# Performance work log

Hardware: AMD Instinct MI355X
Metric: run time of the kernel (lower is better)

Reference implementation:

```python
import jax, jax.numpy as jnp
import numpy as np
import math

B, S, D, H = 2, 2048, 1024, 16
HD = D // H
WINDOW_LEFT = 256   # window_size=(256,-1): only left constraint active
NEG = -1e9


def rotate_half(x):
    x1, x2 = jnp.split(x, 2, axis=-1)
    return jnp.concatenate([-x2, x1], axis=-1)


def setup_inputs() -> dict:
    key = jax.random.key(0)
    ks = jax.random.split(key, 10)
    x = jax.random.normal(ks[0], (B, S, D), dtype=jnp.float32)
    mask = jnp.ones((B, S), dtype=bool)
    cos = jax.random.uniform(ks[1], (B, S, HD), dtype=jnp.float32)
    sin = jax.random.uniform(ks[2], (B, S, HD), dtype=jnp.float32)
    sc = 1.0 / math.sqrt(D)
    Wq = jax.random.normal(ks[3], (D, D), dtype=jnp.float32) * sc
    bq = jax.random.normal(ks[4], (D,), dtype=jnp.float32) * 0.02
    Wk = jax.random.normal(ks[5], (D, D), dtype=jnp.float32) * sc
    Wv = jax.random.normal(ks[6], (D, D), dtype=jnp.float32) * sc
    bv = jax.random.normal(ks[7], (D,), dtype=jnp.float32) * 0.02
    Wo = jax.random.normal(ks[8], (D, D), dtype=jnp.float32) * sc
    bo = jax.random.normal(ks[9], (D,), dtype=jnp.float32) * 0.02
    return {"x": x, "mask": mask, "cos": cos, "sin": sin,
            "Wq": Wq, "bq": bq, "Wk": Wk, "Wv": Wv, "bv": bv,
            "Wo": Wo, "bo": bo}


def reference(x, mask, cos, sin, Wq, bq, Wk, Wv, bv, Wo, bo):
    batch, seq_len, embed_dim = x.shape
    scale = 1.0 / math.sqrt(HD)

    q = x @ Wq + bq          # [b,s,d], bias on q
    k = x @ Wk               # no bias on k
    v = x @ Wv + bv          # bias on v

    def split_heads(t):
        return jnp.swapaxes(t.reshape(batch, seq_len, H, HD), 1, 2)  # [b,h,s,hd]

    q, k, v = split_heads(q), split_heads(k), split_heads(v)

    c = cos[:, None, :, :]   # [b,1,s,hd]
    s_ = sin[:, None, :, :]
    q = q * c + rotate_half(q) * s_
    k = k * c + rotate_half(k) * s_

    scores = jnp.einsum('bhqd,bhkd->bhqk', q, k) * scale
    # padding mask over keys
    scores = jnp.where(mask[:, None, None, :], scores, NEG)
    # causal + sliding-window (left=256) masks combined
    pos = jnp.arange(seq_len)
    rel = pos[None, :] - pos[:, None]          # k - q
    keep = (rel <= 0) & (rel >= -WINDOW_LEFT)  # causal AND window-left
    scores = jnp.where(keep, scores, NEG)

    weights = jax.nn.softmax(scores, axis=-1)
    context = jnp.einsum('bhqk,bhkd->bhqd', weights, v)
    context = jnp.swapaxes(context, 1, 2).reshape(batch, seq_len, embed_dim)
    out = context @ Wo + bo
    out = out * mask[..., None]
    return out
```

## Files before the change

kernel.cpp:

```cpp
#include <hip/hip_runtime.h>
#include <cstdint>
#include <cstddef>

typedef __bf16 bf16;
typedef bf16 bf16x4 __attribute__((ext_vector_type(4)));
typedef bf16 bf16x8 __attribute__((ext_vector_type(8)));
typedef float f32x4 __attribute__((ext_vector_type(4)));

#define S_LEN 2048
#define DIM   1024
#define NHEAD 16
#define HDIM  64

__device__ __forceinline__ f32x4 mfma16(bf16x8 a, bf16x8 b, f32x4 c) {
    return __builtin_amdgcn_mfma_f32_16x16x32_bf16(a, b, c, 0, 0, 0);
}

__device__ __forceinline__ float exp2fast(float x) {
    return __builtin_amdgcn_exp2f(x);
}

__device__ __forceinline__ void gload_lds16(const bf16* g, bf16* l) {
    __builtin_amdgcn_global_load_lds(
        (const __attribute__((address_space(1))) unsigned*)g,
        (__attribute__((address_space(3))) unsigned*)l, 16, 0, 0);
}

__global__ __launch_bounds__(256) void cvt_x_kernel(const float* __restrict__ x,
                                                    bf16* __restrict__ xb) {
    int i = blockIdx.x * 256 + threadIdx.x;
    float4 v = ((const float4*)x)[i];
    bf16x4 o = { (bf16)v.x, (bf16)v.y, (bf16)v.z, (bf16)v.w };
    ((bf16x4*)xb)[i] = o;
}

__global__ __launch_bounds__(256) void wt_kernel(const float* __restrict__ Wq, const float* __restrict__ Wk,
                                                 const float* __restrict__ Wv, const float* __restrict__ Wo,
                                                 bf16* __restrict__ WqT, bf16* __restrict__ WkT,
                                                 bf16* __restrict__ WvT, bf16* __restrict__ WoT) {
    const float* W; bf16* WT;
    int z = blockIdx.z;
    if      (z == 0) { W = Wq; WT = WqT; }
    else if (z == 1) { W = Wk; WT = WkT; }
    else if (z == 2) { W = Wv; WT = WvT; }
    else             { W = Wo; WT = WoT; }
    __shared__ bf16 tile[64][72];
    int k0 = blockIdx.x * 64, n0 = blockIdx.y * 64;
    int t = threadIdx.x;
#pragma unroll
    for (int p = 0; p < 4; ++p) {
        int task = p * 256 + t;
        int ki = task >> 4, nj = (task & 15) * 4;
        float4 v = *(const float4*)(W + (size_t)(k0 + ki) * DIM + n0 + nj);
        tile[ki][nj + 0] = (bf16)v.x; tile[ki][nj + 1] = (bf16)v.y;
        tile[ki][nj + 2] = (bf16)v.z; tile[ki][nj + 3] = (bf16)v.w;
    }
    __syncthreads();
#pragma unroll
    for (int p = 0; p < 4; ++p) {
        int task = p * 256 + t;
        int ni = task >> 4, kj = (task & 15) * 4;
        bf16x4 o = { tile[kj + 0][ni], tile[kj + 1][ni], tile[kj + 2][ni], tile[kj + 3][ni] };
        *(bf16x4*)(WT + (size_t)(n0 + ni) * DIM + k0 + kj) = o;
    }
}

__device__ __forceinline__ void stage_tile(const bf16* __restrict__ A, const bf16* __restrict__ BT,
                                           int m0, int n0, int k0,
                                           bf16* sA, bf16* sB, int w, int lane) {
#pragma unroll
    for (int p = 0; p < 2; ++p) {
        int c = p * 256 + w * 64 + lane;
        const bf16* ga = A + (size_t)(m0 + (c >> 2)) * DIM + k0 + (c & 3) * 8;
        gload_lds16(ga, sA + (p * 256 + w * 64) * 8);
        const bf16* gb = BT + (size_t)(n0 + (c >> 2)) * DIM + k0 + (c & 3) * 8;
        gload_lds16(gb, sB + (p * 256 + w * 64) * 8);
    }
}

__device__ __forceinline__ void gemm_main(const bf16* __restrict__ A, const bf16* __restrict__ BT,
                                          int m0, int n0, f32x4 acc[4][4]) {
    __shared__ bf16 sA[3][128 * 32];
    __shared__ bf16 sB[3][128 * 32];
    int t = threadIdx.x;
    int lane = t & 63, w = t >> 6;
    int wr = w >> 1, wc = w & 1;
    int lc = lane & 15, lr = lane >> 4;
    const int NSTEP = DIM / 32;

    stage_tile(A, BT, m0, n0, 0,  sA[0], sB[0], w, lane);
    stage_tile(A, BT, m0, n0, 32, sA[1], sB[1], w, lane);

    int rs = 0, ss = 2;
    for (int kt = 0; kt < NSTEP; ++kt) {
        if (kt < NSTEP - 1) asm volatile("s_waitcnt vmcnt(4)" ::: "memory");
        else                asm volatile("s_waitcnt vmcnt(0)" ::: "memory");
        __builtin_amdgcn_s_barrier();
        asm volatile("" ::: "memory");
        if (kt < NSTEP - 2)
            stage_tile(A, BT, m0, n0, (kt + 2) * 32, sA[ss], sB[ss], w, lane);

        const bf16* pa = sA[rs] + (wr * 64 + lc) * 32 + lr * 8;
        const bf16* pb = sB[rs] + (wc * 64 + lc) * 32 + lr * 8;
        bf16x8 af[4], bfr[4];
#pragma unroll
        for (int m = 0; m < 4; ++m) af[m] = *(const bf16x8*)(pa + m * 16 * 32);
#pragma unroll
        for (int n = 0; n < 4; ++n) bfr[n] = *(const bf16x8*)(pb + n * 16 * 32);
#pragma unroll
        for (int m = 0; m < 4; ++m)
#pragma unroll
            for (int n = 0; n < 4; ++n)
                acc[m][n] = mfma16(af[m], bfr[n], acc[m][n]);
        rs = (rs == 2) ? 0 : rs + 1;
        ss = (ss == 2) ? 0 : ss + 1;
    }
}

__global__ __launch_bounds__(256, 3) void gemm_qkv_kernel(const bf16* __restrict__ xb,
                                                          const bf16* __restrict__ WqT, const bf16* __restrict__ WkT,
                                                          const bf16* __restrict__ WvT,
                                                          const float* __restrict__ bq, const float* __restrict__ bv,
                                                          const float* __restrict__ cosp, const float* __restrict__ sinp,
                                                          bf16* __restrict__ qT, bf16* __restrict__ kT,
                                                          bf16* __restrict__ vT) {
    int z = blockIdx.z;
    const bf16* BT = (z == 0) ? WqT : (z == 1) ? WkT : WvT;
    int m0 = blockIdx.x * 128, n0 = blockIdx.y * 128;
    f32x4 acc[4][4] = {};
    gemm_main(xb, BT, m0, n0, acc);

    int t = threadIdx.x;
    int lane = t & 63, w = t >> 6;
    int wr = w >> 1, wc = w & 1;
    int lc = lane & 15, lr = lane >> 4;
    int row0 = m0 + wr * 64 + lr * 4;
    int h = (n0 >> 6) + wc;

    if (z < 2) {
        bf16* qkT = (z == 0) ? qT : kT;
#pragma unroll
        for (int nf = 0; nf < 2; ++nf) {
            int hd1 = lc + nf * 16;
            int c1i = h * HDIM + hd1;
            float b1 = (z == 0) ? bq[c1i] : 0.0f;
            float b2 = (z == 0) ? bq[c1i + 32] : 0.0f;
#pragma unroll
            for (int mf = 0; mf < 4; ++mf) {
#pragma unroll
                for (int r = 0; r < 4; ++r) {
                    int bs = row0 + mf * 16 + r;
                    size_t cb = (size_t)bs * HDIM + hd1;
                    float c1 = cosp[cb], s1 = sinp[cb];
                    float c2 = cosp[cb + 32], s2 = sinp[cb + 32];
                    float v1 = acc[mf][nf][r] + b1;
                    float v2 = acc[mf][nf + 2][r] + b2;
                    int b = bs >> 11, s = bs & (S_LEN - 1);
                    size_t o = ((size_t)(b * NHEAD + h) * S_LEN + s) * HDIM;
                    qkT[o + hd1]      = (bf16)(v1 * c1 - v2 * s1);
                    qkT[o + hd1 + 32] = (bf16)(v2 * c2 + v1 * s2);
                }
            }
        }
    } else {
#pragma unroll
        for (int nf = 0; nf < 4; ++nf) {
            int hd = lc + nf * 16;
            float bvv = bv[h * HDIM + hd];
#pragma unroll
            for (int mf = 0; mf < 4; ++mf) {
                bf16x4 o;
#pragma unroll
                for (int r = 0; r < 4; ++r) o[r] = (bf16)(acc[mf][nf][r] + bvv);
                int bs = row0 + mf * 16;
                int b = bs >> 11, s = bs & (S_LEN - 1);
                *(bf16x4*)(vT + ((size_t)((b * NHEAD + h) * HDIM + hd)) * S_LEN + s) = o;
            }
        }
    }
}

__global__ __launch_bounds__(256, 3) void gemm_out_kernel(const bf16* __restrict__ ctx, const bf16* __restrict__ WoT,
                                                          const float* __restrict__ bo, float* __restrict__ out) {
    int m0 = blockIdx.x * 128, n0 = blockIdx.y * 128;
    f32x4 acc[4][4] = {};
    gemm_main(ctx, WoT, m0, n0, acc);
    int t = threadIdx.x;
    int lane = t & 63, w = t >> 6;
    int wr = w >> 1, wc = w & 1;
    int lc = lane & 15, lr = lane >> 4;
    int row0 = m0 + wr * 64 + lr * 4;
    int col0 = n0 + wc * 64 + lc;
#pragma unroll
    for (int nf = 0; nf < 4; ++nf) {
        int col = col0 + nf * 16;
        float bvv = bo[col];
#pragma unroll
        for (int mf = 0; mf < 4; ++mf)
#pragma unroll
            for (int r = 0; r < 4; ++r)
                out[(size_t)(row0 + mf * 16 + r) * DIM + col] = acc[mf][nf][r] + bvv;
    }
}

__global__ __launch_bounds__(64) void attn_kernel(const bf16* __restrict__ qT, const bf16* __restrict__ kT,
                                                  const bf16* __restrict__ vT, bf16* __restrict__ ctx) {
    int q0 = blockIdx.x * 32;
    int bh = blockIdx.y;
    int b = bh >> 4, h = bh & 15;
    int lane = threadIdx.x;
    int lc = lane & 15, lr = lane >> 4;
    __shared__ bf16 sP[32 * 64];
    char* sPb = (char*)sP;
    const bf16* Qb = qT + (size_t)bh * S_LEN * HDIM;
    const bf16* Kb = kT + (size_t)bh * S_LEN * HDIM;
    const bf16* Vb = vT + (size_t)bh * HDIM * S_LEN;

    const float SCL = 0.125f * 1.44269504089f;
    const int swz = (lc & 7) << 4;

    bf16x8 qf[2][2];
#pragma unroll
    for (int mf = 0; mf < 2; ++mf)
#pragma unroll
        for (int kk = 0; kk < 2; ++kk)
            qf[mf][kk] = *(const bf16x8*)(Qb + (size_t)(q0 + mf * 16 + lc) * HDIM + kk * 32 + lr * 8);

    f32x4 accO[2][4] = {};
    float mrun[2] = { -30000.0f, -30000.0f };
    float lrun[2] = { 0.0f, 0.0f };

    int klo = (q0 >= 256) ? ((q0 - 256) >> 6) : 0;
    int khi = (q0 + 31) >> 6;

    bf16x8 kfc[8], kfn[8], vf[8];
#pragma unroll
    for (int nf = 0; nf < 4; ++nf)
#pragma unroll
        for (int kk = 0; kk < 2; ++kk)
            kfc[nf * 2 + kk] = *(const bf16x8*)(Kb + (size_t)(klo * 64 + nf * 16 + lc) * HDIM + kk * 32 + lr * 8);

    for (int kt = klo; kt <= khi; ++kt) {
        int kbase = kt * 64;
#pragma unroll
        for (int n4 = 0; n4 < 4; ++n4)
#pragma unroll
            for (int kk = 0; kk < 2; ++kk)
                vf[n4 * 2 + kk] = *(const bf16x8*)(Vb + (size_t)(n4 * 16 + lc) * S_LEN + kbase + kk * 32 + lr * 8);
        if (kt < khi) {
#pragma unroll
            for (int nf = 0; nf < 4; ++nf)
#pragma unroll
                for (int kk = 0; kk < 2; ++kk)
                    kfn[nf * 2 + kk] = *(const bf16x8*)(Kb + (size_t)(kbase + 64 + nf * 16 + lc) * HDIM + kk * 32 + lr * 8);
        }

        f32x4 sacc[2][4] = {};
        __builtin_amdgcn_s_setprio(1);
#pragma unroll
        for (int nf = 0; nf < 4; ++nf)
#pragma unroll
            for (int kk = 0; kk < 2; ++kk) {
                sacc[0][nf] = mfma16(kfc[nf * 2 + kk], qf[0][kk], sacc[0][nf]);
                sacc[1][nf] = mfma16(kfc[nf * 2 + kk], qf[1][kk], sacc[1][nf]);
            }
        __builtin_amdgcn_s_setprio(0);
#pragma unroll
        for (int mf = 0; mf < 2; ++mf) {
            int qi = q0 + mf * 16 + lc;
#pragma unroll
            for (int nf = 0; nf < 4; ++nf)
#pragma unroll
                for (int r = 0; r < 4; ++r) {
                    int ki = kbase + nf * 16 + lr * 4 + r;
                    bool keep = (ki <= qi) && (ki >= qi - 256);
                    sacc[mf][nf][r] = keep ? sacc[mf][nf][r] * SCL : -30000.0f;
                }
        }
#pragma unroll
        for (int mf = 0; mf < 2; ++mf) {
            float mx = sacc[mf][0][0];
#pragma unroll
            for (int nf = 0; nf < 4; ++nf)
#pragma unroll
                for (int r = 0; r < 4; ++r) mx = fmaxf(mx, sacc[mf][nf][r]);
            mx = fmaxf(mx, __shfl_xor(mx, 16));
            mx = fmaxf(mx, __shfl_xor(mx, 32));
            float mnew = fmaxf(mrun[mf], mx);
            float alpha = exp2fast(mrun[mf] - mnew);
            mrun[mf] = mnew;
            float rsum = 0.0f;
#pragma unroll
            for (int nf = 0; nf < 4; ++nf)
#pragma unroll
                for (int r = 0; r < 4; ++r) {
                    float e = exp2fast(sacc[mf][nf][r] - mnew);
                    sacc[mf][nf][r] = e;
                    rsum += e;
                }
            rsum += __shfl_xor(rsum, 16);
            rsum += __shfl_xor(rsum, 32);
            lrun[mf] = lrun[mf] * alpha + rsum;
            float aq[4];
#pragma unroll
            for (int r = 0; r < 4; ++r) aq[r] = __shfl(alpha, lr * 4 + r);
#pragma unroll
            for (int n4 = 0; n4 < 4; ++n4)
#pragma unroll
                for (int r = 0; r < 4; ++r) accO[mf][n4][r] *= aq[r];
        }
#pragma unroll
        for (int mf = 0; mf < 2; ++mf)
#pragma unroll
            for (int nf = 0; nf < 4; ++nf) {
                bf16x4 o = { (bf16)sacc[mf][nf][0], (bf16)sacc[mf][nf][1],
                             (bf16)sacc[mf][nf][2], (bf16)sacc[mf][nf][3] };
                int wb = ((mf * 16 + lc) * 64 + nf * 16 + lr * 4) * 2;
                *(bf16x4*)(sPb + (wb ^ swz)) = o;
            }
        asm volatile("s_waitcnt lgkmcnt(0)" ::: "memory");
        bf16x8 pf[2][2];
#pragma unroll
        for (int mf = 0; mf < 2; ++mf)
#pragma unroll
            for (int kk = 0; kk < 2; ++kk) {
                int rb = ((mf * 16 + lc) * 64 + kk * 32 + lr * 8) * 2;
                pf[mf][kk] = *(const bf16x8*)(sPb + (rb ^ swz));
            }
        __builtin_amdgcn_s_setprio(1);
#pragma unroll
        for (int n4 = 0; n4 < 4; ++n4)
#pragma unroll
            for (int kk = 0; kk < 2; ++kk) {
                accO[0][n4] = mfma16(pf[0][kk], vf[n4 * 2 + kk], accO[0][n4]);
                accO[1][n4] = mfma16(pf[1][kk], vf[n4 * 2 + kk], accO[1][n4]);
            }
        __builtin_amdgcn_s_setprio(0);
#pragma unroll
        for (int i = 0; i < 8; ++i) kfc[i] = kfn[i];
    }
#pragma unroll
    for (int mf = 0; mf < 2; ++mf) {
        float linv = 1.0f / lrun[mf];
        float lq[4];
#pragma unroll
        for (int r = 0; r < 4; ++r) lq[r] = __shfl(linv, lr * 4 + r);
#pragma unroll
        for (int n4 = 0; n4 < 4; ++n4)
#pragma unroll
            for (int r = 0; r < 4; ++r) {
                int s = q0 + mf * 16 + lr * 4 + r;
                int d = n4 * 16 + lc;
                ctx[((size_t)(b * S_LEN + s)) * DIM + h * HDIM + d] = (bf16)(accO[mf][n4][r] * lq[r]);
            }
    }
}

extern "C" void kernel_launch(void* const* d_in, const int* in_sizes, int n_in,
                              void* d_out, int out_size, void* d_ws, size_t ws_size,
                              hipStream_t stream) {
    const float* x    = (const float*)d_in[0];
    const float* cosp = (const float*)d_in[2];
    const float* sinp = (const float*)d_in[3];
    const float* Wq   = (const float*)d_in[4];
    const float* bq   = (const float*)d_in[5];
    const float* Wk   = (const float*)d_in[6];
    const float* Wv   = (const float*)d_in[7];
    const float* bv   = (const float*)d_in[8];
    const float* Wo   = (const float*)d_in[9];
    const float* bo   = (const float*)d_in[10];
    float* out = (float*)d_out;

    char* ws = (char*)d_ws;
    const size_t MB = 1ull << 20;
    bf16* xb  = (bf16*)(ws + 0 * MB);
    bf16* WqT = (bf16*)(ws + 8 * MB);
    bf16* WkT = (bf16*)(ws + 10 * MB);
    bf16* WvT = (bf16*)(ws + 12 * MB);
    bf16* WoT = (bf16*)(ws + 14 * MB);
    bf16* qT  = (bf16*)(ws + 16 * MB);
    bf16* kT  = (bf16*)(ws + 24 * MB);
    bf16* vT  = (bf16*)(ws + 32 * MB);
    bf16* ctx = (bf16*)(ws + 40 * MB);

    cvt_x_kernel<<<4096, 256, 0, stream>>>(x, xb);
    wt_kernel<<<dim3(16, 16, 4), 256, 0, stream>>>(Wq, Wk, Wv, Wo, WqT, WkT, WvT, WoT);
    gemm_qkv_kernel<<<dim3(32, 8, 3), 256, 0, stream>>>(xb, WqT, WkT, WvT, bq, bv, cosp, sinp, qT, kT, vT);
    attn_kernel<<<dim3(64, 32), 64, 0, stream>>>(qT, kT, vT, ctx);
    gemm_out_kernel<<<dim3(32, 8), 256, 0, stream>>>(ctx, WoT, bo, out);
}
```

Measured before the change: 104.6 us.

## Rewrite QKV GEMM with 256x256 tiles, swizzled LDS and block remap

Replaces the fused QKV projection GEMM's 128x128 tile with 256-thread blocks by a 256x256 tile with 512 threads. It uses a K-step of 64, double-buffered LDS with an XOR swizzle, a remapped 1D grid of 192 blocks, and s_setprio around MFMA bursts. Wq/Wk/Wv are treated as one contiguous transposed weight, which relies on WqT/WkT/WvT sitting adjacent in the workspace. The aim is more data reuse per tile, fewer LDS bank conflicts and better L2 locality. The cost is higher register pressure (128 accumulator floats per thread), a grid smaller than the CU count, and one full wait plus barrier per K step.

Result: no change. 103.9 us (-0.6%).

```diff
diff --git a/kernel.cpp b/kernel.cpp
--- a/kernel.cpp
+++ b/kernel.cpp
@@ -65,88 +65,94 @@
     }
 }
 
-__device__ __forceinline__ void stage_tile(const bf16* __restrict__ A, const bf16* __restrict__ BT,
-                                           int m0, int n0, int k0,
-                                           bf16* sA, bf16* sB, int w, int lane) {
-#pragma unroll
-    for (int p = 0; p < 2; ++p) {
-        int c = p * 256 + w * 64 + lane;
-        const bf16* ga = A + (size_t)(m0 + (c >> 2)) * DIM + k0 + (c & 3) * 8;
-        gload_lds16(ga, sA + (p * 256 + w * 64) * 8);
-        const bf16* gb = BT + (size_t)(n0 + (c >> 2)) * DIM + k0 + (c & 3) * 8;
-        gload_lds16(gb, sB + (p * 256 + w * 64) * 8);
-    }
-}
-
-__device__ __forceinline__ void gemm_main(const bf16* __restrict__ A, const bf16* __restrict__ BT,
-                                          int m0, int n0, f32x4 acc[4][4]) {
-    __shared__ bf16 sA[3][128 * 32];
-    __shared__ bf16 sB[3][128 * 32];
-    int t = threadIdx.x;
-    int lane = t & 63, w = t >> 6;
-    int wr = w >> 1, wc = w & 1;
-    int lc = lane & 15, lr = lane >> 4;
-    const int NSTEP = DIM / 32;
-
-    stage_tile(A, BT, m0, n0, 0,  sA[0], sB[0], w, lane);
-    stage_tile(A, BT, m0, n0, 32, sA[1], sB[1], w, lane);
-
-    int rs = 0, ss = 2;
-    for (int kt = 0; kt < NSTEP; ++kt) {
-        if (kt < NSTEP - 1) asm volatile("s_waitcnt vmcnt(4)" ::: "memory");
-        else                asm volatile("s_waitcnt vmcnt(0)" ::: "memory");
-        __builtin_amdgcn_s_barrier();
-        asm volatile("" ::: "memory");
-        if (kt < NSTEP - 2)
-            stage_tile(A, BT, m0, n0, (kt + 2) * 32, sA[ss], sB[ss], w, lane);
-
-        const bf16* pa = sA[rs] + (wr * 64 + lc) * 32 + lr * 8;
-        const bf16* pb = sB[rs] + (wc * 64 + lc) * 32 + lr * 8;
-        bf16x8 af[4], bfr[4];
-#pragma unroll
-        for (int m = 0; m < 4; ++m) af[m] = *(const bf16x8*)(pa + m * 16 * 32);
-#pragma unroll
-        for (int n = 0; n < 4; ++n) bfr[n] = *(const bf16x8*)(pb + n * 16 * 32);
-#pragma unroll
-        for (int m = 0; m < 4; ++m)
-#pragma unroll
-            for (int n = 0; n < 4; ++n)
-                acc[m][n] = mfma16(af[m], bfr[n], acc[m][n]);
-        rs = (rs == 2) ? 0 : rs + 1;
-        ss = (ss == 2) ? 0 : ss + 1;
-    }
-}
-
-__global__ __launch_bounds__(256, 3) void gemm_qkv_kernel(const bf16* __restrict__ xb,
-                                                          const bf16* __restrict__ WqT, const bf16* __restrict__ WkT,
-                                                          const bf16* __restrict__ WvT,
+__device__ __forceinline__ void stage256(const bf16* __restrict__ A, const bf16* __restrict__ BT,
+                                         int m0, int n0, int k0, int t, int w, bf16* dst) {
+#pragma unroll
+    for (int i = 0; i < 4; ++i) {
+        int c = i * 512 + t;
+        int row = c >> 3;
+        int colb = ((c & 7) * 16) ^ ((row & 7) << 4);
+        gload_lds16(A + (size_t)(m0 + row) * DIM + k0 + (colb >> 1), dst + i * 4096 + w * 512);
+    }
+#pragma unroll
+    for (int i = 0; i < 4; ++i) {
+        int c = i * 512 + t;
+        int row = c >> 3;
+        int colb = ((c & 7) * 16) ^ ((row & 7) << 4);
+        gload_lds16(BT + (size_t)(n0 + row) * DIM + k0 + (colb >> 1), dst + 16384 + i * 4096 + w * 512);
+    }
+}
+
+__global__ __launch_bounds__(512, 2) void gemm_qkv_kernel(const bf16* __restrict__ xb,
+                                                          const bf16* __restrict__ WallT,
                                                           const float* __restrict__ bq, const float* __restrict__ bv,
                                                           const float* __restrict__ cosp, const float* __restrict__ sinp,
                                                           bf16* __restrict__ qT, bf16* __restrict__ kT,
                                                           bf16* __restrict__ vT) {
-    int z = blockIdx.z;
-    const bf16* BT = (z == 0) ? WqT : (z == 1) ? WkT : WvT;
-    int m0 = blockIdx.x * 128, n0 = blockIdx.y * 128;
-    f32x4 acc[4][4] = {};
-    gemm_main(xb, BT, m0, n0, acc);
-
-    int t = threadIdx.x;
-    int lane = t & 63, w = t >> 6;
-    int wr = w >> 1, wc = w & 1;
+    __shared__ bf16 lds[2][32768];
+    int t = threadIdx.x, lane = t & 63, w = t >> 6;
+    int wr = w >> 2, wc = w & 3;
     int lc = lane & 15, lr = lane >> 4;
-    int row0 = m0 + wr * 64 + lr * 4;
-    int h = (n0 >> 6) + wc;
-
+    int bid = blockIdx.x;
+    int swz = (bid & 7) * 24 + (bid >> 3);
+    int bx = swz / 12, by = swz % 12;
+    int m0 = bx * 256, n0 = by * 256;
+
+    f32x4 acc[8][4] = {};
+    const int aswz = (lc & 7) << 4;
+
+    stage256(xb, WallT, m0, n0, 0, t, w, lds[0]);
+    asm volatile("s_waitcnt vmcnt(0)" ::: "memory");
+    __builtin_amdgcn_s_barrier();
+    __builtin_amdgcn_sched_barrier(0);
+
+    const int NT = DIM / 64;
+    for (int kt = 0; kt < NT; ++kt) {
+        if (kt + 1 < NT) stage256(xb, WallT, m0, n0, (kt + 1) * 64, t, w, lds[(kt + 1) & 1]);
+        const char* bufb = (const char*)lds[kt & 1];
+        bf16x8 aF[4], bF[4];
+#pragma unroll
+        for (int ks = 0; ks < 2; ++ks) {
+#pragma unroll
+            for (int nf = 0; nf < 4; ++nf) {
+                int row = wc * 64 + nf * 16 + lc;
+                bF[nf] = *(const bf16x8*)(bufb + 32768 + ((row * 128 + ks * 64 + lr * 16) ^ aswz));
+            }
+#pragma unroll
+            for (int half = 0; half < 2; ++half) {
+#pragma unroll
+                for (int m4 = 0; m4 < 4; ++m4) {
+                    int row = wr * 128 + (half * 4 + m4) * 16 + lc;
+                    aF[m4] = *(const bf16x8*)(bufb + ((row * 128 + ks * 64 + lr * 16) ^ aswz));
+                }
+                __builtin_amdgcn_s_setprio(1);
+#pragma unroll
+                for (int m4 = 0; m4 < 4; ++m4)
+#pragma unroll
+                    for (int nf = 0; nf < 4; ++nf)
+                        acc[half * 4 + m4][nf] = mfma16(aF[m4], bF[nf], acc[half * 4 + m4][nf]);
+                __builtin_amdgcn_s_setprio(0);
+            }
+        }
+        if (kt + 1 < NT) {
+            asm volatile("s_waitcnt vmcnt(0)" ::: "memory");
+            __builtin_amdgcn_s_barrier();
+            __builtin_amdgcn_sched_barrier(0);
+        }
+    }
+
+    int z = by >> 2;
+    int h = (by & 3) * 4 + wc;
+    int row0 = m0 + wr * 128 + lr * 4;
     if (z < 2) {
         bf16* qkT = (z == 0) ? qT : kT;
 #pragma unroll
         for (int nf = 0; nf < 2; ++nf) {
-            int hd1 = lc + nf * 16;
-            int c1i = h * HDIM + hd1;
-            float b1 = (z == 0) ? bq[c1i] : 0.0f;
-            float b2 = (z == 0) ? bq[c1i + 32] : 0.0f;
-#pragma unroll
-            for (int mf = 0; mf < 4; ++mf) {
+            int hd1 = nf * 16 + lc;
+            float b1 = (z == 0) ? bq[h * HDIM + hd1] : 0.0f;
+            float b2 = (z == 0) ? bq[h * HDIM + hd1 + 32] : 0.0f;
+#pragma unroll
+            for (int mf = 0; mf < 8; ++mf) {
 #pragma unroll
                 for (int r = 0; r < 4; ++r) {
                     int bs = row0 + mf * 16 + r;
@@ -165,10 +171,10 @@
     } else {
 #pragma unroll
         for (int nf = 0; nf < 4; ++nf) {
-            int hd = lc + nf * 16;
+            int hd = nf * 16 + lc;
             float bvv = bv[h * HDIM + hd];
 #pragma unroll
-            for (int mf = 0; mf < 4; ++mf) {
+            for (int mf = 0; mf < 8; ++mf) {
                 bf16x4 o;
 #pragma unroll
                 for (int r = 0; r < 4; ++r) o[r] = (bf16)(acc[mf][nf][r] + bvv);
@@ -177,6 +183,58 @@
                 *(bf16x4*)(vT + ((size_t)((b * NHEAD + h) * HDIM + hd)) * S_LEN + s) = o;
             }
         }
+    }
+}
+
+__device__ __forceinline__ void stage_tile(const bf16* __restrict__ A, const bf16* __restrict__ BT,
+                                           int m0, int n0, int k0,
+                                           bf16* sA, bf16* sB, int w, int lane) {
+#pragma unroll
+    for (int p = 0; p < 2; ++p) {
+        int c = p * 256 + w * 64 + lane;
+        const bf16* ga = A + (size_t)(m0 + (c >> 2)) * DIM + k0 + (c & 3) * 8;
+        gload_lds16(ga, sA + (p * 256 + w * 64) * 8);
+        const bf16* gb = BT + (size_t)(n0 + (c >> 2)) * DIM + k0 + (c & 3) * 8;
+        gload_lds16(gb, sB + (p * 256 + w * 64) * 8);
+    }
+}
+
+__device__ __forceinline__ void gemm_main(const bf16* __restrict__ A, const bf16* __restrict__ BT,
+                                          int m0, int n0, f32x4 acc[4][4]) {
+    __shared__ bf16 sA[3][128 * 32];
+    __shared__ bf16 sB[3][128 * 32];
+    int t = threadIdx.x;
+    int lane = t & 63, w = t >> 6;
+    int wr = w >> 1, wc = w & 1;
+    int lc = lane & 15, lr = lane >> 4;
+    const int NSTEP = DIM / 32;
+
+    stage_tile(A, BT, m0, n0, 0,  sA[0], sB[0], w, lane);
+    stage_tile(A, BT, m0, n0, 32, sA[1], sB[1], w, lane);
+
+    int rs = 0, ss = 2;
+    for (int kt = 0; kt < NSTEP; ++kt) {
+        if (kt < NSTEP - 1) asm volatile("s_waitcnt vmcnt(4)" ::: "memory");
+        else                asm volatile("s_waitcnt vmcnt(0)" ::: "memory");
+        __builtin_amdgcn_s_barrier();
+        asm volatile("" ::: "memory");
+        if (kt < NSTEP - 2)
+            stage_tile(A, BT, m0, n0, (kt + 2) * 32, sA[ss], sB[ss], w, lane);
+
+        const bf16* pa = sA[rs] + (wr * 64 + lc) * 32 + lr * 8;
+        const bf16* pb = sB[rs] + (wc * 64 + lc) * 32 + lr * 8;
+        bf16x8 af[4], bfr[4];
+#pragma unroll
+        for (int m = 0; m < 4; ++m) af[m] = *(const bf16x8*)(pa + m * 16 * 32);
+#pragma unroll
+        for (int n = 0; n < 4; ++n) bfr[n] = *(const bf16x8*)(pb + n * 16 * 32);
+#pragma unroll
+        for (int m = 0; m < 4; ++m)
+#pragma unroll
+            for (int n = 0; n < 4; ++n)
+                acc[m][n] = mfma16(af[m], bfr[n], acc[m][n]);
+        rs = (rs == 2) ? 0 : rs + 1;
+        ss = (ss == 2) ? 0 : ss + 1;
     }
 }
 
@@ -385,7 +443,7 @@
 
     cvt_x_kernel<<<4096, 256, 0, stream>>>(x, xb);
     wt_kernel<<<dim3(16, 16, 4), 256, 0, stream>>>(Wq, Wk, Wv, Wo, WqT, WkT, WvT, WoT);
-    gemm_qkv_kernel<<<dim3(32, 8, 3), 256, 0, stream>>>(xb, WqT, WkT, WvT, bq, bv, cosp, sinp, qT, kT, vT);
+    gemm_qkv_kernel<<<192, 512, 0, stream>>>(xb, WqT, bq, bv, cosp, sinp, qT, kT, vT);
     attn_kernel<<<dim3(64, 32), 64, 0, stream>>>(qT, kT, vT, ctx);
     gemm_out_kernel<<<dim3(32, 8), 256, 0, stream>>>(ctx, WoT, bo, out);
 }
```

## Swizzle QKV block order for XCD locality and retile output GEMM to 128x64

Applied to the files above, without the earlier changes.

The QKV GEMM now remaps its linear block id so that the blocks placed on each XCD (bid mod 8) form a contiguous set of output tiles, aiming for better L2 reuse of A and B tiles. The output projection GEMM gets a dedicated 128x64 tile kernel with 2 waves per block and its own triple-buffered LDS staging. This doubles the grid from 256 to 512 blocks so more CUs are busy, and applies the same XCD-aware swizzle. In exchange, each block reuses less data per tile and does more global loads per FLOP.

Result: no change. 106.0 us (+1.4%).

```diff
diff --git a/kernel.cpp b/kernel.cpp
--- a/kernel.cpp
+++ b/kernel.cpp
@@ -124,9 +124,11 @@
                                                           const float* __restrict__ cosp, const float* __restrict__ sinp,
                                                           bf16* __restrict__ qT, bf16* __restrict__ kT,
                                                           bf16* __restrict__ vT) {
-    int z = blockIdx.z;
+    int bid = blockIdx.x + 32 * blockIdx.y + 256 * blockIdx.z;
+    int wg  = (bid & 7) * 96 + (bid >> 3);
+    int z = wg >> 8, rem = wg & 255, by = rem >> 5, bx = rem & 31;
     const bf16* BT = (z == 0) ? WqT : (z == 1) ? WkT : WvT;
-    int m0 = blockIdx.x * 128, n0 = blockIdx.y * 128;
+    int m0 = bx * 128, n0 = by * 128;
     f32x4 acc[4][4] = {};
     gemm_main(xb, BT, m0, n0, acc);
 
@@ -180,20 +182,69 @@
     }
 }
 
-__global__ __launch_bounds__(256, 3) void gemm_out_kernel(const bf16* __restrict__ ctx, const bf16* __restrict__ WoT,
+__device__ __forceinline__ void stage_out(const bf16* __restrict__ A, const bf16* __restrict__ BT,
+                                          int m0, int n0, int k0,
+                                          bf16* sA, bf16* sB, int w, int t) {
+#pragma unroll
+    for (int i = 0; i < 4; ++i) {
+        int c = i * 128 + t;
+        const bf16* ga = A + (size_t)(m0 + (c >> 2)) * DIM + k0 + (c & 3) * 8;
+        gload_lds16(ga, sA + (i * 128 + w * 64) * 8);
+    }
+#pragma unroll
+    for (int i = 0; i < 2; ++i) {
+        int c = i * 128 + t;
+        const bf16* gb = BT + (size_t)(n0 + (c >> 2)) * DIM + k0 + (c & 3) * 8;
+        gload_lds16(gb, sB + (i * 128 + w * 64) * 8);
+    }
+}
+
+__global__ __launch_bounds__(128, 2) void gemm_out_kernel(const bf16* __restrict__ ctx, const bf16* __restrict__ WoT,
                                                           const float* __restrict__ bo, float* __restrict__ out) {
-    int m0 = blockIdx.x * 128, n0 = blockIdx.y * 128;
-    f32x4 acc[4][4] = {};
-    gemm_main(ctx, WoT, m0, n0, acc);
+    __shared__ bf16 sA[3][128 * 32];
+    __shared__ bf16 sB[3][64 * 32];
+    int bid = blockIdx.x + 32 * blockIdx.y;
+    int wg  = (bid & 7) * 64 + (bid >> 3);
+    int bx = wg & 31, by = wg >> 5;
+    int m0 = bx * 128, n0 = by * 64;
     int t = threadIdx.x;
     int lane = t & 63, w = t >> 6;
-    int wr = w >> 1, wc = w & 1;
     int lc = lane & 15, lr = lane >> 4;
-    int row0 = m0 + wr * 64 + lr * 4;
-    int col0 = n0 + wc * 64 + lc;
+    const int NSTEP = DIM / 32;
+
+    f32x4 acc[4][4] = {};
+    stage_out(ctx, WoT, m0, n0, 0,  sA[0], sB[0], w, t);
+    stage_out(ctx, WoT, m0, n0, 32, sA[1], sB[1], w, t);
+
+    int rs = 0, ss = 2;
+    for (int kt = 0; kt < NSTEP; ++kt) {
+        if (kt < NSTEP - 1) asm volatile("s_waitcnt vmcnt(6)" ::: "memory");
+        else                asm volatile("s_waitcnt vmcnt(0)" ::: "memory");
+        __builtin_amdgcn_s_barrier();
+        asm volatile("" ::: "memory");
+        if (kt < NSTEP - 2)
+            stage_out(ctx, WoT, m0, n0, (kt + 2) * 32, sA[ss], sB[ss], w, t);
+
+        const bf16* pa = sA[rs] + (w * 64 + lc) * 32 + lr * 8;
+        const bf16* pb = sB[rs] + lc * 32 + lr * 8;
+        bf16x8 af[4], bfr[4];
+#pragma unroll
+        for (int m = 0; m < 4; ++m) af[m] = *(const bf16x8*)(pa + m * 16 * 32);
+#pragma unroll
+        for (int n = 0; n < 4; ++n) bfr[n] = *(const bf16x8*)(pb + n * 16 * 32);
+#pragma unroll
+        for (int m = 0; m < 4; ++m)
+#pragma unroll
+            for (int n = 0; n < 4; ++n)
+                acc[m][n] = mfma16(af[m], bfr[n], acc[m][n]);
+        rs = (rs == 2) ? 0 : rs + 1;
+        ss = (ss == 2) ? 0 : ss + 1;
+    }
+
+    int row0 = m0 + w * 64 + lr * 4;
 #pragma unroll
     for (int nf = 0; nf < 4; ++nf) {
-        int col = col0 + nf * 16;
+        int col = n0 + lc + nf * 16;
         float bvv = bo[col];
 #pragma unroll
         for (int mf = 0; mf < 4; ++mf)
@@ -387,5 +438,5 @@
     wt_kernel<<<dim3(16, 16, 4), 256, 0, stream>>>(Wq, Wk, Wv, Wo, WqT, WkT, WvT, WoT);
     gemm_qkv_kernel<<<dim3(32, 8, 3), 256, 0, stream>>>(xb, WqT, WkT, WvT, bq, bv, cosp, sinp, qT, kT, vT);
     attn_kernel<<<dim3(64, 32), 64, 0, stream>>>(qT, kT, vT, ctx);
-    gemm_out_kernel<<<dim3(32, 8), 256, 0, stream>>>(ctx, WoT, bo, out);
-}
+    gemm_out_kernel<<<dim3(32, 16), 128, 0, stream>>>(ctx, WoT, bo, out);
+}
```

## Share K/V tiles across four waves via double-buffered LDS staging in attention

Applied to the files above, without the earlier changes.

The attention kernel moves from one 64-thread wave per 32-query block to 256-thread blocks covering 128 queries. K and V tiles are loaded once per block into swizzled LDS with async global-to-LDS loads and double buffering, replacing the per-wave register loads from global memory. Block IDs are remapped so each XCD handles a contiguous set of heads, which is meant to improve L2 locality. In exchange the kernel adds block-wide barriers, and some waves sit idle on tiles outside their own window, which adds work imbalance.

Result: faster. 95.45 us (-8.7%).

```diff
diff --git a/kernel.cpp b/kernel.cpp
--- a/kernel.cpp
+++ b/kernel.cpp
@@ -203,21 +203,33 @@
     }
 }
 
-__global__ __launch_bounds__(64) void attn_kernel(const bf16* __restrict__ qT, const bf16* __restrict__ kT,
-                                                  const bf16* __restrict__ vT, bf16* __restrict__ ctx) {
-    int q0 = blockIdx.x * 32;
-    int bh = blockIdx.y;
+__global__ __launch_bounds__(256, 3) void attn_kernel(const bf16* __restrict__ qT, const bf16* __restrict__ kT,
+                                                      const bf16* __restrict__ vT, bf16* __restrict__ ctx) {
+    int bid = blockIdx.x + 16 * blockIdx.y;
+    int xcd = bid & 7, idx = bid >> 3;
+    int bh = xcd * 4 + (idx >> 4);
+    int qb = idx & 15;
     int b = bh >> 4, h = bh & 15;
-    int lane = threadIdx.x;
+    int t = threadIdx.x, lane = t & 63, w = t >> 6;
     int lc = lane & 15, lr = lane >> 4;
-    __shared__ bf16 sP[32 * 64];
-    char* sPb = (char*)sP;
+
+    __shared__ bf16 sK[2][4096];
+    __shared__ bf16 sV[2][4096];
+    __shared__ bf16 sP[4][2048];
+
     const bf16* Qb = qT + (size_t)bh * S_LEN * HDIM;
     const bf16* Kb = kT + (size_t)bh * S_LEN * HDIM;
     const bf16* Vb = vT + (size_t)bh * HDIM * S_LEN;
 
     const float SCL = 0.125f * 1.44269504089f;
     const int swz = (lc & 7) << 4;
+    char* sPw = (char*)sP[w];
+
+    int q0 = qb * 128 + w * 32;
+    int kt_lo_b = (qb >= 2) ? (qb * 128 - 256) >> 6 : 0;
+    int kt_hi_b = (qb * 128 + 127) >> 6;
+    int klo_w = (q0 >= 256) ? (q0 - 256) >> 6 : 0;
+    int khi_w = (q0 + 31) >> 6;
 
     bf16x8 qf[2][2];
 #pragma unroll
@@ -230,115 +242,130 @@
     float mrun[2] = { -30000.0f, -30000.0f };
     float lrun[2] = { 0.0f, 0.0f };
 
-    int klo = (q0 >= 256) ? ((q0 - 256) >> 6) : 0;
-    int khi = (q0 + 31) >> 6;
-
-    bf16x8 kfc[8], kfn[8], vf[8];
-#pragma unroll
-    for (int nf = 0; nf < 4; ++nf)
-#pragma unroll
-        for (int kk = 0; kk < 2; ++kk)
-            kfc[nf * 2 + kk] = *(const bf16x8*)(Kb + (size_t)(klo * 64 + nf * 16 + lc) * HDIM + kk * 32 + lr * 8);
-
-    for (int kt = klo; kt <= khi; ++kt) {
-        int kbase = kt * 64;
-#pragma unroll
-        for (int n4 = 0; n4 < 4; ++n4)
-#pragma unroll
-            for (int kk = 0; kk < 2; ++kk)
-                vf[n4 * 2 + kk] = *(const bf16x8*)(Vb + (size_t)(n4 * 16 + lc) * S_LEN + kbase + kk * 32 + lr * 8);
-        if (kt < khi) {
-#pragma unroll
-            for (int nf = 0; nf < 4; ++nf)
-#pragma unroll
-                for (int kk = 0; kk < 2; ++kk)
-                    kfn[nf * 2 + kk] = *(const bf16x8*)(Kb + (size_t)(kbase + 64 + nf * 16 + lc) * HDIM + kk * 32 + lr * 8);
+#define STAGE_KV(kt_, s_) {                                                             \
+        int kbase_ = (kt_) * 64;                                                        \
+        _Pragma("unroll")                                                               \
+        for (int p = 0; p < 2; ++p) {                                                   \
+            int c = p * 256 + t;                                                        \
+            int row = c >> 3, ch = c & 7;                                               \
+            int colb = (ch * 16) ^ ((row & 7) << 4);                                    \
+            bf16* dst = (bf16*)&sK[s_][0] + (p * 256 + (t & ~63)) * 8;                  \
+            gload_lds16(Kb + (size_t)(kbase_ + row) * HDIM + (colb >> 1), dst);         \
+            bf16* dsv = (bf16*)&sV[s_][0] + (p * 256 + (t & ~63)) * 8;                  \
+            gload_lds16(Vb + (size_t)row * S_LEN + kbase_ + (colb >> 1), dsv);          \
+        }                                                                               \
+    }
+
+    STAGE_KV(kt_lo_b, 0);
+    if (kt_lo_b + 1 <= kt_hi_b) STAGE_KV(kt_lo_b + 1, 1);
+
+    for (int kt = kt_lo_b; kt <= kt_hi_b; ++kt) {
+        int s = (kt - kt_lo_b) & 1;
+        if (kt < kt_hi_b) asm volatile("s_waitcnt vmcnt(4)" ::: "memory");
+        else              asm volatile("s_waitcnt vmcnt(0)" ::: "memory");
+        __builtin_amdgcn_s_barrier();
+        asm volatile("" ::: "memory");
+
+        if (kt >= klo_w && kt <= khi_w) {
+            int kbase = kt * 64;
+            const char* kb = (const char*)&sK[s][0];
+            const char* vb = (const char*)&sV[s][0];
+
+            f32x4 sacc[2][4] = {};
+            __builtin_amdgcn_s_setprio(1);
+#pragma unroll
+            for (int nf = 0; nf < 4; ++nf) {
+                int key = nf * 16 + lc;
+#pragma unroll
+                for (int kk = 0; kk < 2; ++kk) {
+                    bf16x8 kf = *(const bf16x8*)(kb + key * 128 + ((kk * 64 + lr * 16) ^ swz));
+                    sacc[0][nf] = mfma16(kf, qf[0][kk], sacc[0][nf]);
+                    sacc[1][nf] = mfma16(kf, qf[1][kk], sacc[1][nf]);
+                }
+            }
+            __builtin_amdgcn_s_setprio(0);
+#pragma unroll
+            for (int mf = 0; mf < 2; ++mf) {
+                int qi = q0 + mf * 16 + lc;
+#pragma unroll
+                for (int nf = 0; nf < 4; ++nf)
+#pragma unroll
+                    for (int r = 0; r < 4; ++r) {
+                        int ki = kbase + nf * 16 + lr * 4 + r;
+                        bool keep = (ki <= qi) && (ki >= qi - 256);
+                        sacc[mf][nf][r] = keep ? sacc[mf][nf][r] * SCL : -30000.0f;
+                    }
+            }
+#pragma unroll
+            for (int mf = 0; mf < 2; ++mf) {
+                float mx = sacc[mf][0][0];
+#pragma unroll
+                for (int nf = 0; nf < 4; ++nf)
+#pragma unroll
+                    for (int r = 0; r < 4; ++r) mx = fmaxf(mx, sacc[mf][nf][r]);
+                mx = fmaxf(mx, __shfl_xor(mx, 16));
+                mx = fmaxf(mx, __shfl_xor(mx, 32));
+                float mnew = fmaxf(mrun[mf], mx);
+                float alpha = exp2fast(mrun[mf] - mnew);
+                mrun[mf] = mnew;
+                float rsum = 0.0f;
+#pragma unroll
+                for (int nf = 0; nf < 4; ++nf)
+#pragma unroll
+                    for (int r = 0; r < 4; ++r) {
+                        float e = exp2fast(sacc[mf][nf][r] - mnew);
+                        sacc[mf][nf][r] = e;
+                        rsum += e;
+                    }
+                rsum += __shfl_xor(rsum, 16);
+                rsum += __shfl_xor(rsum, 32);
+                lrun[mf] = lrun[mf] * alpha + rsum;
+                float aq[4];
+#pragma unroll
+                for (int r = 0; r < 4; ++r) aq[r] = __shfl(alpha, lr * 4 + r);
+#pragma unroll
+                for (int n4 = 0; n4 < 4; ++n4)
+#pragma unroll
+                    for (int r = 0; r < 4; ++r) accO[mf][n4][r] *= aq[r];
+            }
+#pragma unroll
+            for (int mf = 0; mf < 2; ++mf)
+#pragma unroll
+                for (int nf = 0; nf < 4; ++nf) {
+                    bf16x4 o = { (bf16)sacc[mf][nf][0], (bf16)sacc[mf][nf][1],
+                                 (bf16)sacc[mf][nf][2], (bf16)sacc[mf][nf][3] };
+                    int wb = ((mf * 16 + lc) * 64 + nf * 16 + lr * 4) * 2;
+                    *(bf16x4*)(sPw + (wb ^ swz)) = o;
+                }
+            asm volatile("s_waitcnt lgkmcnt(0)" ::: "memory");
+            bf16x8 pf[2][2];
+#pragma unroll
+            for (int mf = 0; mf < 2; ++mf)
+#pragma unroll
+                for (int kk = 0; kk < 2; ++kk) {
+                    int rb = ((mf * 16 + lc) * 64 + kk * 32 + lr * 8) * 2;
+                    pf[mf][kk] = *(const bf16x8*)(sPw + (rb ^ swz));
+                }
+            __builtin_amdgcn_s_setprio(1);
+#pragma unroll
+            for (int n4 = 0; n4 < 4; ++n4) {
+                int d = n4 * 16 + lc;
+#pragma unroll
+                for (int kk = 0; kk < 2; ++kk) {
+                    bf16x8 vf = *(const bf16x8*)(vb + d * 128 + ((kk * 64 + lr * 16) ^ swz));
+                    accO[0][n4] = mfma16(pf[0][kk], vf, accO[0][n4]);
+                    accO[1][n4] = mfma16(pf[1][kk], vf, accO[1][n4]);
+                }
+            }
+            __builtin_amdgcn_s_setprio(0);
         }
 
-        f32x4 sacc[2][4] = {};
-        __builtin_amdgcn_s_setprio(1);
-#pragma unroll
-        for (int nf = 0; nf < 4; ++nf)
-#pragma unroll
-            for (int kk = 0; kk < 2; ++kk) {
-                sacc[0][nf] = mfma16(kfc[nf * 2 + kk], qf[0][kk], sacc[0][nf]);
-                sacc[1][nf] = mfma16(kfc[nf * 2 + kk], qf[1][kk], sacc[1][nf]);
-            }
-        __builtin_amdgcn_s_setprio(0);
-#pragma unroll
-        for (int mf = 0; mf < 2; ++mf) {
-            int qi = q0 + mf * 16 + lc;
-#pragma unroll
-            for (int nf = 0; nf < 4; ++nf)
-#pragma unroll
-                for (int r = 0; r < 4; ++r) {
-                    int ki = kbase + nf * 16 + lr * 4 + r;
-                    bool keep = (ki <= qi) && (ki >= qi - 256);
-                    sacc[mf][nf][r] = keep ? sacc[mf][nf][r] * SCL : -30000.0f;
-                }
-        }
-#pragma unroll
-        for (int mf = 0; mf < 2; ++mf) {
-            float mx = sacc[mf][0][0];
-#pragma unroll
-            for (int nf = 0; nf < 4; ++nf)
-#pragma unroll
-                for (int r = 0; r < 4; ++r) mx = fmaxf(mx, sacc[mf][nf][r]);
-            mx = fmaxf(mx, __shfl_xor(mx, 16));
-            mx = fmaxf(mx, __shfl_xor(mx, 32));
-            float mnew = fmaxf(mrun[mf], mx);
-            float alpha = exp2fast(mrun[mf] - mnew);
-            mrun[mf] = mnew;
-            float rsum = 0.0f;
-#pragma unroll
-            for (int nf = 0; nf < 4; ++nf)
-#pragma unroll
-                for (int r = 0; r < 4; ++r) {
-                    float e = exp2fast(sacc[mf][nf][r] - mnew);
-                    sacc[mf][nf][r] = e;
-                    rsum += e;
-                }
-            rsum += __shfl_xor(rsum, 16);
-            rsum += __shfl_xor(rsum, 32);
-            lrun[mf] = lrun[mf] * alpha + rsum;
-            float aq[4];
-#pragma unroll
-            for (int r = 0; r < 4; ++r) aq[r] = __shfl(alpha, lr * 4 + r);
-#pragma unroll
-            for (int n4 = 0; n4 < 4; ++n4)
-#pragma unroll
-                for (int r = 0; r < 4; ++r) accO[mf][n4][r] *= aq[r];
-        }
-#pragma unroll
-        for (int mf = 0; mf < 2; ++mf)
-#pragma unroll
-            for (int nf = 0; nf < 4; ++nf) {
-                bf16x4 o = { (bf16)sacc[mf][nf][0], (bf16)sacc[mf][nf][1],
-                             (bf16)sacc[mf][nf][2], (bf16)sacc[mf][nf][3] };
-                int wb = ((mf * 16 + lc) * 64 + nf * 16 + lr * 4) * 2;
-                *(bf16x4*)(sPb + (wb ^ swz)) = o;
-            }
-        asm volatile("s_waitcnt lgkmcnt(0)" ::: "memory");
-        bf16x8 pf[2][2];
-#pragma unroll
-        for (int mf = 0; mf < 2; ++mf)
-#pragma unroll
-            for (int kk = 0; kk < 2; ++kk) {
-                int rb = ((mf * 16 + lc) * 64 + kk * 32 + lr * 8) * 2;
-                pf[mf][kk] = *(const bf16x8*)(sPb + (rb ^ swz));
-            }
-        __builtin_amdgcn_s_setprio(1);
-#pragma unroll
-        for (int n4 = 0; n4 < 4; ++n4)
-#pragma unroll
-            for (int kk = 0; kk < 2; ++kk) {
-                accO[0][n4] = mfma16(pf[0][kk], vf[n4 * 2 + kk], accO[0][n4]);
-                accO[1][n4] = mfma16(pf[1][kk], vf[n4 * 2 + kk], accO[1][n4]);
-            }
-        __builtin_amdgcn_s_setprio(0);
-#pragma unroll
-        for (int i = 0; i < 8; ++i) kfc[i] = kfn[i];
-    }
+        __builtin_amdgcn_s_barrier();
+        asm volatile("" ::: "memory");
+        if (kt + 2 <= kt_hi_b) STAGE_KV(kt + 2, s);
+    }
+#undef STAGE_KV
+
 #pragma unroll
     for (int mf = 0; mf < 2; ++mf) {
         float linv = 1.0f / lrun[mf];
@@ -386,6 +413,6 @@
     cvt_x_kernel<<<4096, 256, 0, stream>>>(x, xb);
     wt_kernel<<<dim3(16, 16, 4), 256, 0, stream>>>(Wq, Wk, Wv, Wo, WqT, WkT, WvT, WoT);
     gemm_qkv_kernel<<<dim3(32, 8, 3), 256, 0, stream>>>(xb, WqT, WkT, WvT, bq, bv, cosp, sinp, qT, kT, vT);
-    attn_kernel<<<dim3(64, 32), 64, 0, stream>>>(qT, kT, vT, ctx);
+    attn_kernel<<<dim3(16, 32), 256, 0, stream>>>(qT, kT, vT, ctx);
     gemm_out_kernel<<<dim3(32, 8), 256, 0, stream>>>(ctx, WoT, bo, out);
 }
```
